# Kernel optimization log

Hardware: AMD Instinct MI355X
Metric: run time of the kernel (lower is better)

## Reference

```python
import jax, jax.numpy as jnp
import numpy as np

H = 512      # hidden_size (hardcoded in __init__)
WD = 1024    # word_dim (hardcoded)
V = 4096     # len(i2w)+4
B, S, T = 256, 80, 28


def setup_inputs() -> dict:
    key = jax.random.key(0)
    ks = jax.random.split(key, 14)

    def gl(k, shape, fan_in):
        return (jax.random.normal(k, shape, jnp.float32) / np.sqrt(fan_in)).astype(jnp.float32)

    return {
        "encoder_last_hidden_state": jax.random.normal(ks[0], (1, B, H), jnp.float32),
        "encoder_output": jax.random.normal(ks[1], (B, S, H), jnp.float32),
        "targets": jax.random.randint(ks[2], (B, T), 0, V, dtype=jnp.int32),
        # embedding table
        "embedding": gl(ks[3], (V, WD), WD),
        # attention MLP (4 stacked linears, no activations, per the source)
        "W1": gl(ks[4], (2 * H, H), 2 * H), "b1": jnp.zeros((H,), jnp.float32),
        "W2": gl(ks[5], (H, H), H), "b2": jnp.zeros((H,), jnp.float32),
        "W3": gl(ks[6], (H, H), H), "b3": jnp.zeros((H,), jnp.float32),
        "W4": gl(ks[7], (H, H), H), "b4": jnp.zeros((H,), jnp.float32),
        "Ww": gl(ks[8], (H, 1), H),
        # GRU (input = hidden_size + word_dim = 1536), PyTorch gate order r,z,n
        "W_ih": gl(ks[9], (3 * H, H + WD), H + WD), "b_ih": jnp.zeros((3 * H,), jnp.float32),
        "W_hh": gl(ks[10], (3 * H, H), H), "b_hh": jnp.zeros((3 * H,), jnp.float32),
        # output projection
        "Wo": gl(ks[11], (H, V), H), "bo": jnp.zeros((V,), jnp.float32),
    }


def reference(encoder_last_hidden_state, encoder_output, targets, embedding,
              W1, b1, W2, b2, W3, b3, W4, b4, Ww,
              W_ih, b_ih, W_hh, b_hh, Wo, bo):
    n_steps = targets.shape[1] - 1  # seq_len - 1 decode steps

    def attention(h, enc):
        # h: (B,H) decoder hidden; enc: (B,S,H)
        hs = jnp.broadcast_to(h[:, None, :], enc.shape)
        m = jnp.concatenate([enc, hs], axis=-1)          # (B,S,2H)
        x = m @ W1 + b1
        x = x @ W2 + b2
        x = x @ W3 + b3
        x = x @ W4 + b4
        attw = jax.nn.softmax((x @ Ww)[..., 0], axis=1)  # (B,S)
        return jnp.einsum('bs,bsh->bh', attw, enc)       # context (B,H)

    def gru_cell(x, h):
        gi = x @ W_ih.T + b_ih
        gh = h @ W_hh.T + b_hh
        ir, iz, inn = jnp.split(gi, 3, axis=-1)
        hr, hz, hn = jnp.split(gh, 3, axis=-1)
        r = jax.nn.sigmoid(ir + hr)
        z = jax.nn.sigmoid(iz + hz)
        n = jnp.tanh(inn + r * hn)
        return (1.0 - z) * n + z * h

    h0 = encoder_last_hidden_state[0]                    # (B,H)
    w0 = jnp.ones((encoder_output.shape[0],), jnp.int32) # <BOS> = 1

    def step(carry, _):
        h, w = carry
        emb = embedding[w]                               # (B,WD)
        ctx = attention(h, encoder_output)               # (B,H)
        x = jnp.concatenate([emb, ctx], axis=-1)         # (B,WD+H)
        hn = gru_cell(x, h)
        logits = hn @ Wo + bo                            # (B,V)
        wn = jnp.argmax(logits, axis=-1).astype(jnp.int32)
        return (hn, wn), logits

    _, logits_seq = jax.lax.scan(step, (h0, w0), None, length=n_steps)
    seq_logProb = jnp.swapaxes(logits_seq, 0, 1)         # (B, T-1, V)
    seq_predictions = jnp.argmax(seq_logProb, axis=-1)
    return seq_logProb, seq_predictions
```

## Files before the change

### kernel.cpp

```cpp
#include <hip/hip_runtime.h>

#define B_ 256
#define S_ 80
#define H_ 512
#define V_ 4096
#define NSTEP 27

typedef unsigned short u16;
typedef __attribute__((ext_vector_type(8))) short short8v;
typedef __attribute__((ext_vector_type(4))) float f32x4;
typedef __attribute__((ext_vector_type(4))) unsigned short ushort4v;

#define MFMA_(a,b,c) __builtin_amdgcn_mfma_f32_16x16x32_bf16(a,b,c,0,0,0)
#define MFMA3(acc, ah, al, bh, bl) do{ acc = MFMA_(ah,bh,acc); acc = MFMA_(ah,bl,acc); acc = MFMA_(al,bh,acc);}while(0)

__device__ __forceinline__ unsigned fkey(float v){
    unsigned u = __float_as_uint(v);
    return (u & 0x80000000u) ? ~u : (u | 0x80000000u);
}
__device__ __forceinline__ u16 bf16_rne(float f){
    unsigned u = __float_as_uint(f);
    return (u16)((u + 0x7FFFu + ((u >> 16) & 1u)) >> 16);
}
__device__ __forceinline__ void split_f4(float4 v, ushort4v& hi, ushort4v& lo){
    float arr[4] = {v.x, v.y, v.z, v.w};
    ushort4v h, l;
#pragma unroll
    for (int i = 0; i < 4; ++i){
        u16 hb = bf16_rne(arr[i]);
        h[i] = hb;
        l[i] = bf16_rne(arr[i] - __uint_as_float(((unsigned)hb) << 16));
    }
    hi = h; lo = l;
}

__global__ __launch_bounds__(64) void matvec512(const float* __restrict__ W,
                                                const float* __restrict__ v,
                                                float* __restrict__ out){
    int row = blockIdx.x, lane = threadIdx.x;
    const float* wr = W + row * 512;
    float s = 0.f;
#pragma unroll
    for (int i = 0; i < 8; ++i) s += wr[lane + 64*i] * v[lane + 64*i];
#pragma unroll
    for (int off = 32; off; off >>= 1) s += __shfl_xor(s, off);
    if (lane == 0) out[row] = s;
}

__global__ __launch_bounds__(256) void prep_all(
    const float* __restrict__ Whh, const float* __restrict__ Wo,
    const float* __restrict__ emb, const float* __restrict__ Wih,
    const float* __restrict__ elhs,
    u16* __restrict__ WhhHi, u16* __restrict__ WhhLo,
    u16* __restrict__ WoThi, u16* __restrict__ WoTlo,
    u16* __restrict__ EmbHi, u16* __restrict__ EmbLo,
    u16* __restrict__ WihLHi, u16* __restrict__ WihLLo,
    u16* __restrict__ Sh, u16* __restrict__ Sl,
    unsigned* __restrict__ zp, int nz)
{
    __shared__ float T[64][65];
    int b = blockIdx.x, tid = threadIdx.x;
    if (b < 768){
        int idx = (b*256 + tid)*4;
        float4 v = *(const float4*)&Whh[idx];
        ushort4v h,l; split_f4(v,h,l);
        *(ushort4v*)&WhhHi[idx]=h; *(ushort4v*)&WhhLo[idx]=l;
    } else if (b < 1280){
        int lb = b - 768;
        int k0 = (lb & 7)*64, n0 = (lb >> 3)*64;
#pragma unroll
        for (int i = 0; i < 16; ++i){
            int idx = tid + i*256;
            int kk = idx >> 6, nn = idx & 63;
            T[kk][nn] = Wo[(size_t)(k0+kk)*4096 + n0+nn];
        }
        __syncthreads();
#pragma unroll
        for (int i = 0; i < 16; ++i){
            int idx = tid + i*256;
            int nn = idx >> 6, kk = idx & 63;
            float v = T[kk][nn];
            u16 hi = bf16_rne(v);
            u16 lo = bf16_rne(v - __uint_as_float(((unsigned)hi) << 16));
            size_t o = (size_t)(n0+nn)*512 + k0+kk;
            WoThi[o] = hi; WoTlo[o] = lo;
        }
    } else if (b < 5376){
        int idx = ((b-1280)*256 + tid)*4;
        float4 v = *(const float4*)&emb[idx];
        ushort4v h,l; split_f4(v,h,l);
        *(ushort4v*)&EmbHi[idx]=h; *(ushort4v*)&EmbLo[idx]=l;
    } else if (b < 6912){
        int id = ((b-5376)*256 + tid)*4;
        int r = id >> 10, c = id & 1023;
        float4 v = *(const float4*)&Wih[(size_t)r*1536 + c];
        ushort4v h,l; split_f4(v,h,l);
        *(ushort4v*)&WihLHi[id]=h; *(ushort4v*)&WihLLo[id]=l;
    } else if (b < 7040){
        int idx = ((b-6912)*256 + tid)*4;
        float4 v = *(const float4*)&elhs[idx];
        ushort4v h,l; split_f4(v,h,l);
        *(ushort4v*)&Sh[idx]=h; *(ushort4v*)&Sl[idx]=l;
    } else {
        int i = ((b-7040)*256 + tid)*4;
        if (i < nz){ zp[i]=0u; zp[i+1]=0u; zp[i+2]=0u; zp[i+3]=0u; }
    }
}

__global__ __launch_bounds__(512) void attn_ctx(const float* __restrict__ enc,
                                                const float* __restrict__ weff,
                                                float* __restrict__ ctx){
    __shared__ float att[S_];
    int b = blockIdx.x, tid = threadIdx.x;
    int wv = tid >> 6, lane = tid & 63;
    float w8[8];
#pragma unroll
    for (int i = 0; i < 8; ++i) w8[i] = weff[lane + 64*i];
    const float* eb = enc + (size_t)b * (S_*H_);
    for (int s = wv; s < S_; s += 8){
        const float* e = eb + s*512;
        float acc = 0.f;
#pragma unroll
        for (int i = 0; i < 8; ++i) acc += e[lane + 64*i] * w8[i];
#pragma unroll
        for (int off = 32; off; off >>= 1) acc += __shfl_xor(acc, off);
        if (lane == 0) att[s] = acc;
    }
    __syncthreads();
    if (tid == 0){
        float mx = att[0];
        for (int s = 1; s < S_; ++s) mx = fmaxf(mx, att[s]);
        float sum = 0.f;
        for (int s = 0; s < S_; ++s){ float e = expf(att[s] - mx); att[s] = e; sum += e; }
        float inv = 1.f / sum;
        for (int s = 0; s < S_; ++s) att[s] *= inv;
    }
    __syncthreads();
    float a = 0.f;
    for (int s = 0; s < S_; ++s) a += att[s] * eb[s*512 + tid];
    ctx[b*512 + tid] = a;
}

__device__ __forceinline__ void step_mm_body(char* smem, int m0, int nt, int n_logits,
    const u16* __restrict__ Ahg, const u16* __restrict__ Alg,
    const u16* __restrict__ WoHi, const u16* __restrict__ WoLo,
    const u16* __restrict__ WhhHi, const u16* __restrict__ WhhLo,
    const float* __restrict__ bo,
    float* __restrict__ logits, unsigned long long* __restrict__ Pcur,
    float* __restrict__ gh_out)
{
    u16 (*Ah)[2048] = (u16(*)[2048])(smem);
    u16 (*Al)[2048] = (u16(*)[2048])(smem + 8192);
    u16 (*Bh)[2048] = (u16(*)[2048])(smem + 16384);
    u16 (*Bl)[2048] = (u16(*)[2048])(smem + 24576);
    bool isL = nt < n_logits;
    int nbase = (isL ? nt : nt - n_logits) * 64;
    const u16* Bhg = isL ? WoHi : WhhHi;
    const u16* Blg = isL ? WoLo : WhhLo;
    int tid = threadIdx.x, lane = tid & 63, wid = tid >> 6;
    int wy = wid & 1, wx = wid >> 1;
    int l15 = lane & 15, rg = lane >> 4, lk = rg * 8;
    int sr = tid >> 2, sk8 = (tid & 3) * 8;

    const u16* gAh = Ahg + (size_t)(m0 + sr)*512 + sk8;
    const u16* gAl = Alg + (size_t)(m0 + sr)*512 + sk8;
    const u16* gBh = Bhg + (size_t)(nbase + sr)*512 + sk8;
    const u16* gBl = Blg + (size_t)(nbase + sr)*512 + sk8;

    *(short8v*)&Ah[0][tid*8] = *(const short8v*)gAh;
    *(short8v*)&Al[0][tid*8] = *(const short8v*)gAl;
    *(short8v*)&Bh[0][tid*8] = *(const short8v*)gBh;
    *(short8v*)&Bl[0][tid*8] = *(const short8v*)gBl;
    short8v r1a = *(const short8v*)(gAh + 32), r1b = *(const short8v*)(gAl + 32);
    short8v r1c = *(const short8v*)(gBh + 32), r1d = *(const short8v*)(gBl + 32);
    short8v r2a = *(const short8v*)(gAh + 64), r2b = *(const short8v*)(gAl + 64);
    short8v r2c = *(const short8v*)(gBh + 64), r2d = *(const short8v*)(gBl + 64);
    __syncthreads();

    f32x4 acc[2][2] = {};
    int p = 0;
    for (int k0 = 0; k0 < 512; k0 += 32){
        if (k0 + 32 < 512){
            *(short8v*)&Ah[p^1][tid*8] = r1a;
            *(short8v*)&Al[p^1][tid*8] = r1b;
            *(short8v*)&Bh[p^1][tid*8] = r1c;
            *(short8v*)&Bl[p^1][tid*8] = r1d;
            r1a = r2a; r1b = r2b; r1c = r2c; r1d = r2d;
            if (k0 + 96 < 512){
                r2a = *(const short8v*)(gAh + k0 + 96);
                r2b = *(const short8v*)(gAl + k0 + 96);
                r2c = *(const short8v*)(gBh + k0 + 96);
                r2d = *(const short8v*)(gBl + k0 + 96);
            }
        }
        short8v afh0 = *(const short8v*)&Ah[p][(wy*32 +  0 + l15)*32 + lk];
        short8v afh1 = *(const short8v*)&Ah[p][(wy*32 + 16 + l15)*32 + lk];
        short8v afl0 = *(const short8v*)&Al[p][(wy*32 +  0 + l15)*32 + lk];
        short8v afl1 = *(const short8v*)&Al[p][(wy*32 + 16 + l15)*32 + lk];
        short8v bfh0 = *(const short8v*)&Bh[p][(wx*32 +  0 + l15)*32 + lk];
        short8v bfh1 = *(const short8v*)&Bh[p][(wx*32 + 16 + l15)*32 + lk];
        short8v bfl0 = *(const short8v*)&Bl[p][(wx*32 +  0 + l15)*32 + lk];
        short8v bfl1 = *(const short8v*)&Bl[p][(wx*32 + 16 + l15)*32 + lk];
        MFMA3(acc[0][0], afh0, afl0, bfh0, bfl0);
        MFMA3(acc[0][1], afh0, afl0, bfh1, bfl1);
        MFMA3(acc[1][0], afh1, afl1, bfh0, bfl0);
        MFMA3(acc[1][1], afh1, afl1, bfh1, bfl1);
        __syncthreads();
        p ^= 1;
    }

    int col0 = nbase + wx*32 + l15;
    if (isL){
        float bo0 = bo[col0], bo1 = bo[col0 + 16];
#pragma unroll
        for (int mf = 0; mf < 2; ++mf){
#pragma unroll
            for (int r = 0; r < 4; ++r){
                int row = m0 + wy*32 + mf*16 + rg*4 + r;
                float v0 = acc[mf][0][r] + bo0;
                float v1 = acc[mf][1][r] + bo1;
                float* crow = logits + (size_t)row * (NSTEP * (size_t)V_);
                crow[col0]      = v0;
                crow[col0 + 16] = v1;
                unsigned long long k0_ = ((unsigned long long)fkey(v0) << 32) | (unsigned)(4095 - col0);
                unsigned long long k1_ = ((unsigned long long)fkey(v1) << 32) | (unsigned)(4095 - (col0+16));
                unsigned long long best = k0_ > k1_ ? k0_ : k1_;
#pragma unroll
                for (int off = 1; off < 16; off <<= 1){
                    unsigned long long o = __shfl_xor(best, off);
                    if (o > best) best = o;
                }
                if (l15 == 0) atomicMax(&Pcur[row], best);
            }
        }
    } else {
#pragma unroll
        for (int mf = 0; mf < 2; ++mf)
#pragma unroll
            for (int r = 0; r < 4; ++r){
                int row = m0 + wy*32 + mf*16 + rg*4 + r;
                gh_out[(size_t)row*1536 + col0]      = acc[mf][0][r];
                gh_out[(size_t)row*1536 + col0 + 16] = acc[mf][1][r];
            }
    }
}

__global__ __launch_bounds__(256) void front3(
    const u16* __restrict__ EmbHi, const u16* __restrict__ EmbLo,
    const u16* __restrict__ WihLHi, const u16* __restrict__ WihLLo,
    float* __restrict__ Eproj,
    const float* __restrict__ ctx, const float* __restrict__ WihR,
    const float* __restrict__ bih, float* __restrict__ gictx,
    const u16* __restrict__ Sh0, const u16* __restrict__ Sl0,
    const u16* __restrict__ WhhHi, const u16* __restrict__ WhhLo,
    float* __restrict__ gh0)
{
    __shared__ __align__(16) char smem[32768];
    int b = blockIdx.x, tid = threadIdx.x;
    if (b < 384){
        int bn = b % 12, bm = b / 12;
        int n0 = bn * 128, m0 = bm * 128;
        int lane = tid & 63, wid = tid >> 6;
        int wy = wid & 1, wx = wid >> 1;
        int l15 = lane & 15, rg = lane >> 4, lk = rg * 8;
        u16* Ah = (u16*)smem;
        u16* Al = (u16*)(smem + 8192);
        u16* Bh = (u16*)(smem + 16384);
        u16* Bl = (u16*)(smem + 24576);
        const u16* gA[2][2]; const u16* gB[2][2];
#pragma unroll
        for (int j = 0; j < 2; ++j){
            int s = tid + j*256;
            int row = s >> 2, k8 = (s & 3)*8;
            gA[0][j] = EmbHi + (size_t)(m0+row)*1024 + k8;
            gA[1][j] = EmbLo + (size_t)(m0+row)*1024 + k8;
            gB[0][j] = WihLHi + (size_t)(n0+row)*1024 + k8;
            gB[1][j] = WihLLo + (size_t)(n0+row)*1024 + k8;
        }
        short8v rA[2][2], rB[2][2];
#pragma unroll
        for (int h = 0; h < 2; ++h)
#pragma unroll
            for (int j = 0; j < 2; ++j){
                rA[h][j] = *(const short8v*)gA[h][j];
                rB[h][j] = *(const short8v*)gB[h][j];
            }
        f32x4 acc[4][4] = {};
        for (int k0 = 0; k0 < 1024; k0 += 32){
            __syncthreads();
#pragma unroll
            for (int j = 0; j < 2; ++j){
                int s8 = (tid + j*256)*8;
                *(short8v*)&Ah[s8] = rA[0][j];
                *(short8v*)&Al[s8] = rA[1][j];
                *(short8v*)&Bh[s8] = rB[0][j];
                *(short8v*)&Bl[s8] = rB[1][j];
            }
            __syncthreads();
            if (k0 + 32 < 1024){
#pragma unroll
                for (int h = 0; h < 2; ++h)
#pragma unroll
                    for (int j = 0; j < 2; ++j){
                        rA[h][j] = *(const short8v*)(gA[h][j] + k0 + 32);
                        rB[h][j] = *(const short8v*)(gB[h][j] + k0 + 32);
                    }
            }
            short8v afh[4], afl[4];
#pragma unroll
            for (int mf = 0; mf < 4; ++mf){
                afh[mf] = *(const short8v*)&Ah[(wy*64 + mf*16 + l15)*32 + lk];
                afl[mf] = *(const short8v*)&Al[(wy*64 + mf*16 + l15)*32 + lk];
            }
#pragma unroll
            for (int nf = 0; nf < 4; ++nf){
                short8v bfh = *(const short8v*)&Bh[(wx*64 + nf*16 + l15)*32 + lk];
                short8v bfl = *(const short8v*)&Bl[(wx*64 + nf*16 + l15)*32 + lk];
#pragma unroll
                for (int mf = 0; mf < 4; ++mf)
                    MFMA3(acc[mf][nf], afh[mf], afl[mf], bfh, bfl);
            }
        }
        int col0 = n0 + wx*64 + l15;
#pragma unroll
        for (int mf = 0; mf < 4; ++mf)
#pragma unroll
            for (int r = 0; r < 4; ++r){
                int row = m0 + wy*64 + mf*16 + rg*4 + r;
#pragma unroll
                for (int nf = 0; nf < 4; ++nf)
                    Eproj[(size_t)row*1536 + col0 + nf*16] = acc[mf][nf][r];
            }
    } else if (b < 576){
        int lb = b - 384;
        int m0 = (lb & 7) * 32, n0 = (lb >> 3) * 64;
        float (*As)[36] = (float(*)[36])smem;
        float (*Bs)[68] = (float(*)[68])(smem + 2304);
        int lk = tid & 15, lr = tid >> 4;
        int tx = tid & 15, ty = tid >> 4;
        float c[2][4] = {};
        for (int k0 = 0; k0 < 512; k0 += 16){
#pragma unroll
            for (int i = 0; i < 2; ++i)
                As[lk][lr*2 + i] = ctx[(size_t)(m0 + lr*2 + i)*512 + k0 + lk];
#pragma unroll
            for (int i = 0; i < 4; ++i)
                Bs[lk][lr*4 + i] = WihR[(size_t)(n0 + lr*4 + i)*1536 + k0 + lk];
            __syncthreads();
#pragma unroll
            for (int k = 0; k < 16; ++k){
                float b4[4];
                *(float4*)b4 = *(const float4*)&Bs[k][tx*4];
#pragma unroll
                for (int i = 0; i < 2; ++i){
                    float a = As[k][ty*2 + i];
#pragma unroll
                    for (int j = 0; j < 4; ++j) c[i][j] += a * b4[j];
                }
            }
            __syncthreads();
        }
#pragma unroll
        for (int j = 0; j < 4; ++j){
            float bb = bih[n0 + tx*4 + j];
#pragma unroll
            for (int i = 0; i < 2; ++i)
                gictx[(size_t)(m0 + ty*2 + i)*1536 + n0 + tx*4 + j] = c[i][j] + bb;
        }
    } else {
        int lb = b - 576;
        step_mm_body(smem, (lb & 3)*64, lb >> 2, 0,
                     Sh0, Sl0, nullptr, nullptr, WhhHi, WhhLo,
                     nullptr, nullptr, nullptr, gh0);
    }
}

__global__ __launch_bounds__(128) void gru_pointwise(
    const float* __restrict__ gh, const float* __restrict__ Eproj,
    const float* __restrict__ gictx, const float* __restrict__ bhh,
    const float* __restrict__ hprev, float* __restrict__ hnext,
    u16* __restrict__ Sh, u16* __restrict__ Sl,
    const unsigned long long* __restrict__ Pprev,
    float* __restrict__ preds, int t)
{
    int tid = threadIdx.x;
    int row = blockIdx.x;
    int jj = tid * 4;
    int w = 1;
    if (t > 0){
        w = 4095 - (int)(Pprev[row] & 0xFFFFFFFFull);
        if (w < 0) w = 0; if (w > 4095) w = 4095;
        if (tid == 0) preds[row*NSTEP + (t-1)] = (float)w;
    }
    const float* gr = gh + (size_t)row * 1536;
    const float* ep = Eproj + (size_t)w * 1536;
    const float* gc = gictx + (size_t)row * 1536;
    float4 g0 = *(const float4*)&gr[jj];
    float4 g1 = *(const float4*)&gr[512 + jj];
    float4 g2 = *(const float4*)&gr[1024 + jj];
    float4 e0 = *(const float4*)&ep[jj];
    float4 e1 = *(const float4*)&ep[512 + jj];
    float4 e2 = *(const float4*)&ep[1024 + jj];
    float4 c0 = *(const float4*)&gc[jj];
    float4 c1 = *(const float4*)&gc[512 + jj];
    float4 c2 = *(const float4*)&gc[1024 + jj];
    float4 b0 = *(const float4*)&bhh[jj];
    float4 b1 = *(const float4*)&bhh[512 + jj];
    float4 b2 = *(const float4*)&bhh[1024 + jj];
    float4 ho = *(const float4*)&hprev[(size_t)row*512 + jj];
    const float* G0 = (const float*)&g0; const float* G1 = (const float*)&g1;
    const float* G2 = (const float*)&g2;
    const float* E0 = (const float*)&e0; const float* E1 = (const float*)&e1;
    const float* E2 = (const float*)&e2;
    const float* C0 = (const float*)&c0; const float* C1 = (const float*)&c1;
    const float* C2 = (const float*)&c2;
    const float* B0 = (const float*)&b0; const float* B1 = (const float*)&b1;
    const float* B2 = (const float*)&b2;
    const float* HO = (const float*)&ho;
    float4 res;
    float* R = (float*)&res;
#pragma unroll
    for (int i = 0; i < 4; ++i){
        float gir = E0[i] + C0[i] + G0[i] + B0[i];
        float giz = E1[i] + C1[i] + G1[i] + B1[i];
        float gin = E2[i] + C2[i];
        float rr = 1.f / (1.f + expf(-gir));
        float zz = 1.f / (1.f + expf(-giz));
        float nn = tanhf(gin + rr * (G2[i] + B2[i]));
        R[i] = (1.f - zz)*nn + zz*HO[i];
    }
    size_t o = (size_t)row*512 + jj;
    *(float4*)&hnext[o] = res;
    ushort4v h4, l4; split_f4(res, h4, l4);
    *(ushort4v*)&Sh[o] = h4;
    *(ushort4v*)&Sl[o] = l4;
}

__global__ __launch_bounds__(256) void step_mm(
    const u16* __restrict__ Ahg, const u16* __restrict__ Alg,
    const u16* __restrict__ WoHi, const u16* __restrict__ WoLo,
    const u16* __restrict__ WhhHi, const u16* __restrict__ WhhLo,
    const float* __restrict__ bo,
    float* __restrict__ logits, unsigned long long* __restrict__ Pcur,
    float* __restrict__ gh_out, int n_logits)
{
    __shared__ __align__(16) char smem[32768];
    step_mm_body(smem, blockIdx.x * 64, blockIdx.y, n_logits,
                 Ahg, Alg, WoHi, WoLo, WhhHi, WhhLo, bo, logits, Pcur, gh_out);
}

__global__ __launch_bounds__(256) void final_pred(const unsigned long long* __restrict__ P,
                                                  float* __restrict__ preds){
    int b = threadIdx.x;
    int w = 4095 - (int)(P[b] & 0xFFFFFFFFull);
    if (w < 0) w = 0; if (w > 4095) w = 4095;
    preds[b*NSTEP + (NSTEP-1)] = (float)w;
}

extern "C" void kernel_launch(void* const* d_in, const int* in_sizes, int n_in,
                              void* d_out, int out_size, void* d_ws, size_t ws_size,
                              hipStream_t stream){
    const float* elhs = (const float*)d_in[0];
    const float* enc  = (const float*)d_in[1];
    const float* emb  = (const float*)d_in[3];
    const float* W1   = (const float*)d_in[4];
    const float* W2   = (const float*)d_in[6];
    const float* W3   = (const float*)d_in[8];
    const float* W4   = (const float*)d_in[10];
    const float* Ww   = (const float*)d_in[12];
    const float* Wih  = (const float*)d_in[13];
    const float* bih  = (const float*)d_in[14];
    const float* Whh  = (const float*)d_in[15];
    const float* bhh  = (const float*)d_in[16];
    const float* Wo   = (const float*)d_in[17];
    const float* bo   = (const float*)d_in[18];

    float* out = (float*)d_out;
    float* preds = out + (size_t)B_ * NSTEP * V_;

    float* ws = (float*)d_ws;
    float* Eproj  = ws;  ws += (size_t)V_ * 1536;
    float* gictx  = ws;  ws += (size_t)B_ * 1536;
    float* ctx    = ws;  ws += B_ * H_;
    float* t1     = ws;  ws += 512;
    float* t2     = ws;  ws += 512;
    float* weff   = ws;  ws += 512;
    float* Hf     = ws;  ws += 2 * B_ * H_;
    float* ghbuf  = ws;  ws += B_ * 1536;
    u16* WoT_hi = (u16*)ws;  ws += (size_t)V_ * 512 / 2;
    u16* WoT_lo = (u16*)ws;  ws += (size_t)V_ * 512 / 2;
    u16* WhhHi  = (u16*)ws;  ws += 1536 * 512 / 2;
    u16* WhhLo  = (u16*)ws;  ws += 1536 * 512 / 2;
    u16* Sh     = (u16*)ws;  ws += B_ * H_ / 2;
    u16* Sl     = (u16*)ws;  ws += B_ * H_ / 2;
    unsigned long long* P = (unsigned long long*)ws;

    u16* EmbHi  = (u16*)d_out;
    u16* EmbLo  = EmbHi + (size_t)V_*1024;
    u16* WihLHi = EmbLo + (size_t)V_*1024;
    u16* WihLLo = WihLHi + (size_t)1536*1024;

    prep_all<<<7054, 256, 0, stream>>>(Whh, Wo, emb, Wih, elhs,
                                       WhhHi, WhhLo, WoT_hi, WoT_lo,
                                       EmbHi, EmbLo, WihLHi, WihLLo,
                                       Sh, Sl, (unsigned*)P, NSTEP*256*2);
    matvec512<<<512, 64, 0, stream>>>(W4, Ww, t1);
    matvec512<<<512, 64, 0, stream>>>(W3, t1, t2);
    matvec512<<<512, 64, 0, stream>>>(W2, t2, t1);
    matvec512<<<512, 64, 0, stream>>>(W1, t1, weff);
    attn_ctx<<<B_, 512, 0, stream>>>(enc, weff, ctx);
    front3<<<672, 256, 0, stream>>>(EmbHi, EmbLo, WihLHi, WihLLo, Eproj,
                                    ctx, Wih + 1024, bih, gictx,
                                    Sh, Sl, WhhHi, WhhLo, ghbuf);

    for (int t = 0; t < NSTEP; ++t){
        const float* hr = (t == 0) ? elhs : (Hf + (size_t)((t-1) & 1) * (B_*H_));
        float*       hw = Hf + (size_t)(t & 1) * (B_*H_);
        const unsigned long long* Pprev = P + (size_t)(t > 0 ? t-1 : 0) * 256;
        gru_pointwise<<<256, 128, 0, stream>>>(ghbuf, Eproj, gictx, bhh, hr, hw,
                                               Sh, Sl, Pprev, preds, t);
        dim3 g(4, 64 + 24);
        step_mm<<<g, 256, 0, stream>>>(Sh, Sl, WoT_hi, WoT_lo, WhhHi, WhhLo, bo,
                                       out + (size_t)t * V_, P + (size_t)t*256, ghbuf, 64);
    }
    final_pred<<<1, 256, 0, stream>>>(P + (size_t)(NSTEP-1)*256, preds);
}
```

Measured before the change: 737.4 us.

## Fuse GRU pointwise update into step_mm tail via grid-wide atomic ticket barrier

Drops the separate per-step gru_pointwise launch. Each step_mm block, and each front3 block for step 0, increments an atomic ticket when it finishes; the last block sets a flag. A subset of 32 blocks spins on that flag and then computes the GRU update, the next hidden state and its bf16 hi/lo split for the following step. This removes 27 kernel launches and their gaps from the serial decode loop. In exchange it relies on a spin-wait barrier that assumes the grid is co-resident, and it puts the pointwise work on only 32 blocks.

```diff
diff --git a/kernel.cpp b/kernel.cpp
--- a/kernel.cpp
+++ b/kernel.cpp
@@ -141,6 +141,65 @@
     ctx[b*512 + tid] = a;
 }
 
+__device__ __forceinline__ void gru_tail(int g, int tid, int t,
+    const float* __restrict__ gh, const float* __restrict__ Eproj,
+    const float* __restrict__ gictx, const float* __restrict__ bhh,
+    const float* __restrict__ hprev, float* __restrict__ hnext,
+    u16* __restrict__ Sh, u16* __restrict__ Sl,
+    const unsigned long long* __restrict__ Pcur, float* __restrict__ preds)
+{
+    int r = g*8 + (tid >> 5);
+    int c0 = (tid & 31) * 16;
+    int w = 1;
+    if (t >= 0){
+        w = 4095 - (int)(Pcur[r] & 0xFFFFFFFFull);
+        if (w < 0) w = 0; if (w > 4095) w = 4095;
+        if ((tid & 31) == 0) preds[r*NSTEP + t] = (float)w;
+    }
+    const float* gr = gh + (size_t)r * 1536;
+    const float* ep = Eproj + (size_t)w * 1536;
+    const float* gc = gictx + (size_t)r * 1536;
+    const float* hp = hprev + (size_t)r * 512;
+#pragma unroll
+    for (int j = 0; j < 4; ++j){
+        int c = c0 + j*4;
+        float4 g0 = *(const float4*)&gr[c];
+        float4 g1 = *(const float4*)&gr[512 + c];
+        float4 g2 = *(const float4*)&gr[1024 + c];
+        float4 e0 = *(const float4*)&ep[c];
+        float4 e1 = *(const float4*)&ep[512 + c];
+        float4 e2 = *(const float4*)&ep[1024 + c];
+        float4 q0 = *(const float4*)&gc[c];
+        float4 q1 = *(const float4*)&gc[512 + c];
+        float4 q2 = *(const float4*)&gc[1024 + c];
+        float4 b0 = *(const float4*)&bhh[c];
+        float4 b1 = *(const float4*)&bhh[512 + c];
+        float4 b2 = *(const float4*)&bhh[1024 + c];
+        float4 ho = *(const float4*)&hp[c];
+        const float *G0=(const float*)&g0, *G1=(const float*)&g1, *G2=(const float*)&g2;
+        const float *E0=(const float*)&e0, *E1=(const float*)&e1, *E2=(const float*)&e2;
+        const float *C0=(const float*)&q0, *C1=(const float*)&q1, *C2=(const float*)&q2;
+        const float *B0=(const float*)&b0, *B1=(const float*)&b1, *B2=(const float*)&b2;
+        const float *HO=(const float*)&ho;
+        float4 res; float* R = (float*)&res;
+#pragma unroll
+        for (int i = 0; i < 4; ++i){
+            float gir = E0[i] + C0[i] + G0[i] + B0[i];
+            float giz = E1[i] + C1[i] + G1[i] + B1[i];
+            float gin = E2[i] + C2[i];
+            float rr = 1.f / (1.f + expf(-gir));
+            float zz = 1.f / (1.f + expf(-giz));
+            float nn = tanhf(gin + rr * (G2[i] + B2[i]));
+            R[i] = (1.f - zz)*nn + zz*HO[i];
+        }
+        size_t o = (size_t)r*512 + c;
+        *(float4*)&hnext[o] = res;
+        ushort4v h4, l4; split_f4(res, h4, l4);
+        *(ushort4v*)&Sh[o] = h4;
+        *(ushort4v*)&Sl[o] = l4;
+    }
+}
+
 __device__ __forceinline__ void step_mm_body(char* smem, int m0, int nt, int n_logits,
     const u16* __restrict__ Ahg, const u16* __restrict__ Alg,
     const u16* __restrict__ WoHi, const u16* __restrict__ WoLo,
@@ -253,7 +312,10 @@
     const float* __restrict__ bih, float* __restrict__ gictx,
     const u16* __restrict__ Sh0, const u16* __restrict__ Sl0,
     const u16* __restrict__ WhhHi, const u16* __restrict__ WhhLo,
-    float* __restrict__ gh0)
+    float* __restrict__ gh0,
+    const float* __restrict__ bhh, const float* __restrict__ elhs,
+    float* __restrict__ hn0, u16* __restrict__ ShW, u16* __restrict__ SlW,
+    unsigned* __restrict__ tkt, unsigned* __restrict__ flg)
 {
     __shared__ __align__(16) char smem[32768];
     int b = blockIdx.x, tid = threadIdx.x;
@@ -373,67 +435,22 @@
                      Sh0, Sl0, nullptr, nullptr, WhhHi, WhhLo,
                      nullptr, nullptr, nullptr, gh0);
     }
-}
-
-__global__ __launch_bounds__(128) void gru_pointwise(
-    const float* __restrict__ gh, const float* __restrict__ Eproj,
-    const float* __restrict__ gictx, const float* __restrict__ bhh,
-    const float* __restrict__ hprev, float* __restrict__ hnext,
-    u16* __restrict__ Sh, u16* __restrict__ Sl,
-    const unsigned long long* __restrict__ Pprev,
-    float* __restrict__ preds, int t)
-{
-    int tid = threadIdx.x;
-    int row = blockIdx.x;
-    int jj = tid * 4;
-    int w = 1;
-    if (t > 0){
-        w = 4095 - (int)(Pprev[row] & 0xFFFFFFFFull);
-        if (w < 0) w = 0; if (w > 4095) w = 4095;
-        if (tid == 0) preds[row*NSTEP + (t-1)] = (float)w;
-    }
-    const float* gr = gh + (size_t)row * 1536;
-    const float* ep = Eproj + (size_t)w * 1536;
-    const float* gc = gictx + (size_t)row * 1536;
-    float4 g0 = *(const float4*)&gr[jj];
-    float4 g1 = *(const float4*)&gr[512 + jj];
-    float4 g2 = *(const float4*)&gr[1024 + jj];
-    float4 e0 = *(const float4*)&ep[jj];
-    float4 e1 = *(const float4*)&ep[512 + jj];
-    float4 e2 = *(const float4*)&ep[1024 + jj];
-    float4 c0 = *(const float4*)&gc[jj];
-    float4 c1 = *(const float4*)&gc[512 + jj];
-    float4 c2 = *(const float4*)&gc[1024 + jj];
-    float4 b0 = *(const float4*)&bhh[jj];
-    float4 b1 = *(const float4*)&bhh[512 + jj];
-    float4 b2 = *(const float4*)&bhh[1024 + jj];
-    float4 ho = *(const float4*)&hprev[(size_t)row*512 + jj];
-    const float* G0 = (const float*)&g0; const float* G1 = (const float*)&g1;
-    const float* G2 = (const float*)&g2;
-    const float* E0 = (const float*)&e0; const float* E1 = (const float*)&e1;
-    const float* E2 = (const float*)&e2;
-    const float* C0 = (const float*)&c0; const float* C1 = (const float*)&c1;
-    const float* C2 = (const float*)&c2;
-    const float* B0 = (const float*)&b0; const float* B1 = (const float*)&b1;
-    const float* B2 = (const float*)&b2;
-    const float* HO = (const float*)&ho;
-    float4 res;
-    float* R = (float*)&res;
-#pragma unroll
-    for (int i = 0; i < 4; ++i){
-        float gir = E0[i] + C0[i] + G0[i] + B0[i];
-        float giz = E1[i] + C1[i] + G1[i] + B1[i];
-        float gin = E2[i] + C2[i];
-        float rr = 1.f / (1.f + expf(-gir));
-        float zz = 1.f / (1.f + expf(-giz));
-        float nn = tanhf(gin + rr * (G2[i] + B2[i]));
-        R[i] = (1.f - zz)*nn + zz*HO[i];
-    }
-    size_t o = (size_t)row*512 + jj;
-    *(float4*)&hnext[o] = res;
-    ushort4v h4, l4; split_f4(res, h4, l4);
-    *(ushort4v*)&Sh[o] = h4;
-    *(ushort4v*)&Sl[o] = l4;
+    __syncthreads();
+    if (tid == 0){
+        __threadfence();
+        unsigned my = __hip_atomic_fetch_add(tkt, 1u, __ATOMIC_ACQ_REL, __HIP_MEMORY_SCOPE_AGENT);
+        if (my == 671u) __hip_atomic_store(flg, 1u, __ATOMIC_RELEASE, __HIP_MEMORY_SCOPE_AGENT);
+    }
+    if (b >= 576 && b < 608){
+        int g = b - 576;
+        if (tid == 0){
+            while (__hip_atomic_load(flg, __ATOMIC_ACQUIRE, __HIP_MEMORY_SCOPE_AGENT) == 0u)
+                __builtin_amdgcn_s_sleep(32);
+        }
+        __syncthreads();
+        gru_tail(g, tid, -1, gh0, Eproj, gictx, bhh, elhs, hn0, ShW, SlW,
+                 nullptr, nullptr);
+    }
 }
 
 __global__ __launch_bounds__(256) void step_mm(
@@ -442,11 +459,36 @@
     const u16* __restrict__ WhhHi, const u16* __restrict__ WhhLo,
     const float* __restrict__ bo,
     float* __restrict__ logits, unsigned long long* __restrict__ Pcur,
-    float* __restrict__ gh_out, int n_logits)
+    float* __restrict__ gh_out, int n_logits,
+    const float* __restrict__ Eproj, const float* __restrict__ gictx,
+    const float* __restrict__ bhh,
+    const float* __restrict__ hprevT, float* __restrict__ hnextT,
+    u16* __restrict__ ShW, u16* __restrict__ SlW,
+    float* __restrict__ preds, int t,
+    unsigned* __restrict__ tkt, unsigned* __restrict__ flg, int do_tail)
 {
     __shared__ __align__(16) char smem[32768];
     step_mm_body(smem, blockIdx.x * 64, blockIdx.y, n_logits,
                  Ahg, Alg, WoHi, WoLo, WhhHi, WhhLo, bo, logits, Pcur, gh_out);
+    if (!do_tail) return;
+    int tid = threadIdx.x;
+    __syncthreads();
+    if (tid == 0){
+        __threadfence();
+        unsigned my = __hip_atomic_fetch_add(tkt, 1u, __ATOMIC_ACQ_REL, __HIP_MEMORY_SCOPE_AGENT);
+        if (my == 351u) __hip_atomic_store(flg, 1u, __ATOMIC_RELEASE, __HIP_MEMORY_SCOPE_AGENT);
+    }
+    int nt = blockIdx.y;
+    if (nt >= n_logits && nt < n_logits + 8){
+        int g = (nt - n_logits)*4 + blockIdx.x;
+        if (tid == 0){
+            while (__hip_atomic_load(flg, __ATOMIC_ACQUIRE, __HIP_MEMORY_SCOPE_AGENT) == 0u)
+                __builtin_amdgcn_s_sleep(32);
+        }
+        __syncthreads();
+        gru_tail(g, tid, t, gh_out, Eproj, gictx, bhh, hprevT, hnextT,
+                 ShW, SlW, Pcur, preds);
+    }
 }
 
 __global__ __launch_bounds__(256) void final_pred(const unsigned long long* __restrict__ P,
@@ -494,6 +536,12 @@
     u16* Sh     = (u16*)ws;  ws += B_ * H_ / 2;
     u16* Sl     = (u16*)ws;  ws += B_ * H_ / 2;
     unsigned long long* P = (unsigned long long*)ws;
+    unsigned* aux = (unsigned*)(P + NSTEP*256);
+    unsigned* tickets = aux;
+    unsigned* flags   = aux + 32;
+    unsigned* tkt0    = aux + 64;
+    unsigned* flg0    = aux + 65;
+    const int NZ = NSTEP*256*2 + 66;
 
     u16* EmbHi  = (u16*)d_out;
     u16* EmbLo  = EmbHi + (size_t)V_*1024;
@@ -503,7 +551,7 @@
     prep_all<<<7054, 256, 0, stream>>>(Whh, Wo, emb, Wih, elhs,
                                        WhhHi, WhhLo, WoT_hi, WoT_lo,
                                        EmbHi, EmbLo, WihLHi, WihLLo,
-                                       Sh, Sl, (unsigned*)P, NSTEP*256*2);
+                                       Sh, Sl, (unsigned*)P, NZ);
     matvec512<<<512, 64, 0, stream>>>(W4, Ww, t1);
     matvec512<<<512, 64, 0, stream>>>(W3, t1, t2);
     matvec512<<<512, 64, 0, stream>>>(W2, t2, t1);
@@ -511,17 +559,16 @@
     attn_ctx<<<B_, 512, 0, stream>>>(enc, weff, ctx);
     front3<<<672, 256, 0, stream>>>(EmbHi, EmbLo, WihLHi, WihLLo, Eproj,
                                     ctx, Wih + 1024, bih, gictx,
-                                    Sh, Sl, WhhHi, WhhLo, ghbuf);
+                                    Sh, Sl, WhhHi, WhhLo, ghbuf,
+                                    bhh, elhs, Hf, Sh, Sl, tkt0, flg0);
 
     for (int t = 0; t < NSTEP; ++t){
-        const float* hr = (t == 0) ? elhs : (Hf + (size_t)((t-1) & 1) * (B_*H_));
-        float*       hw = Hf + (size_t)(t & 1) * (B_*H_);
-        const unsigned long long* Pprev = P + (size_t)(t > 0 ? t-1 : 0) * 256;
-        gru_pointwise<<<256, 128, 0, stream>>>(ghbuf, Eproj, gictx, bhh, hr, hw,
-                                               Sh, Sl, Pprev, preds, t);
         dim3 g(4, 64 + 24);
         step_mm<<<g, 256, 0, stream>>>(Sh, Sl, WoT_hi, WoT_lo, WhhHi, WhhLo, bo,
-                                       out + (size_t)t * V_, P + (size_t)t*256, ghbuf, 64);
+            out + (size_t)t * V_, P + (size_t)t*256, ghbuf, 64,
+            Eproj, gictx, bhh,
+            Hf + (size_t)(t & 1) * (B_*H_), Hf + (size_t)((t+1) & 1) * (B_*H_),
+            Sh, Sl, preds, t, tickets + t, flags + t, (t < NSTEP-1) ? 1 : 0);
     }
     final_pred<<<1, 256, 0, stream>>>(P + (size_t)(NSTEP-1)*256, preds);
 }
```

Result: slower. 1.319 ms (+78.9%).
